# Kernel tuning notes

Hardware: AMD Instinct MI355X
Metric: run time of the kernel (lower is better)

The kernel has to match this reference:

```python
import jax, jax.numpy as jnp
import numpy as np

N, D, U = 8192, 512, 256

def setup_inputs() -> dict:
    key = jax.random.key(0)
    ks = jax.random.split(key, 5)
    s = 0.02
    return {
        "x": jax.random.normal(ks[0], (N, D), dtype=jnp.float32),
        "W_q": jax.random.normal(ks[1], (D, U), dtype=jnp.float32) * s,
        "W_k": jax.random.normal(ks[2], (D, U), dtype=jnp.float32) * s,
        "W_v": jax.random.normal(ks[3], (D, U), dtype=jnp.float32) * s,
        "W_o": jax.random.normal(ks[4], (U, D), dtype=jnp.float32) * s,
    }

def reference(x, W_q, W_k, W_v, W_o):
    # x: [N, d]; attention over the sample (batch) dimension
    units = W_q.shape[-1]
    Q = x @ W_q            # [N, U]
    Km = x @ W_k           # [N, U]
    V = x @ W_v            # [N, U]
    scale = 1.0 / jnp.sqrt(jnp.asarray(units, dtype=x.dtype))
    scores = jax.nn.softmax((Q @ Km.T) * scale, axis=-1)  # [N, N]
    return (scores @ V) @ W_o  # [N, d]
```

## Files before the change

kernel.cpp:

```cpp
#include <hip/hip_runtime.h>
#include <stdint.h>


#define N_ 8192
#define D_ 512
#define U_ 256

typedef __attribute__((ext_vector_type(8))) short short8;
typedef __attribute__((ext_vector_type(4))) float f32x4;
typedef __attribute__((ext_vector_type(16))) float f32x16;
typedef __attribute__((ext_vector_type(4))) unsigned int u32x4;
typedef __attribute__((ext_vector_type(2))) unsigned int u32x2;
typedef __attribute__((ext_vector_type(2))) unsigned int uint2v;

#define EXP2F(x) __builtin_amdgcn_exp2f(x)

static __device__ __forceinline__ unsigned short f2bf(float f) {
    union { float f; unsigned int u; } c; c.f = f;
    unsigned int u = c.u;
    u += 0x7FFFu + ((u >> 16) & 1u);
    return (unsigned short)(u >> 16);
}
static __device__ __forceinline__ float bf2f(unsigned int h) {
    union { unsigned int u; float f; } c; c.u = h << 16;
    return c.f;
}
static __device__ __forceinline__ unsigned int cvtpk(float lo, float hi) {
    unsigned int d;
    asm("v_cvt_pk_bf16_f32 %0, %1, %2" : "=v"(d) : "v"(lo), "v"(hi));
    return d;
}

__global__ void k_convert(const float* __restrict__ x, const float* __restrict__ Wq,
                          const float* __restrict__ Wk, const float* __restrict__ Wv,
                          const float* __restrict__ Wo,
                          unsigned short* __restrict__ Wt, unsigned short* __restrict__ Wot,
                          unsigned short* __restrict__ xb) {
    const int b = blockIdx.x, t = threadIdx.x;
    if (b < 2048) {
        int i = (b * 256 + t) * 8;
        f32x4 a = *(const f32x4*)(x + i);
        f32x4 c = *(const f32x4*)(x + i + 4);
        u32x4 o;
        o[0] = cvtpk(a[0], a[1]); o[1] = cvtpk(a[2], a[3]);
        o[2] = cvtpk(c[0], c[1]); o[3] = cvtpk(c[2], c[3]);
        *(u32x4*)(xb + i) = o;
    } else {
        int idx = (b - 2048) * 256 + t;
        if (idx < 768 * 512) {
            int j = idx >> 9, d = idx & 511;
            int which = j >> 8, u = j & 255;
            const float* W = (which == 0) ? Wq : ((which == 1) ? Wk : Wv);
            float v = W[d * 256 + u];
            if (which == 0) v *= 0.0625f * 1.4426950408889634f;
            Wt[idx] = f2bf(v);
        } else {
            int i2 = idx - 768 * 512;
            int jj = i2 >> 8, u = i2 & 255;
            Wot[i2] = f2bf(Wo[u * 512 + jj]);
        }
    }
}

__global__ __launch_bounds__(256) void k_qkv(const unsigned short* __restrict__ xb,
        const unsigned short* __restrict__ Wt,
        unsigned short* __restrict__ Q, unsigned short* __restrict__ K,
        unsigned short* __restrict__ Vt) {
    __shared__ __align__(16) char lds[65536];

    const int t = threadIdx.x;
    const int w = t >> 6, l = t & 63;
    const int lg = l >> 4, ln = l & 15;
    const int bm = blockIdx.x * 128;
    const int j0 = blockIdx.y * 128;

    const int r8 = t >> 3, c8 = t & 7;
    const char* gA = (const char*)xb + (size_t)bm * 1024;
    const char* gB = (const char*)Wt + (size_t)j0 * 1024;

    auto stage = [&](int ks, int b) {
        const char* ga = gA + ks * 128;
        const char* gb = gB + ks * 128;
        char* la = lds + b * 16384;
        char* lb = lds + 32768 + b * 16384;
#pragma unroll
        for (int i = 0; i < 4; ++i) {
            int row = i * 32 + r8;
            int so = row * 1024 + ((c8 ^ (row & 7)) << 4);
            __builtin_amdgcn_global_load_lds(
                (const __attribute__((address_space(1))) void*)(ga + so),
                (__attribute__((address_space(3))) void*)(la + (i * 256 + t) * 16), 16, 0, 0);
            __builtin_amdgcn_global_load_lds(
                (const __attribute__((address_space(1))) void*)(gb + so),
                (__attribute__((address_space(3))) void*)(lb + (i * 256 + t) * 16), 16, 0, 0);
        }
    };

    f32x4 acc[2][8] = {};
    stage(0, 0);
    for (int ks = 0; ks < 8; ++ks) {
        const int buf = ks & 1;
        __syncthreads();
        if (ks + 1 < 8) stage(ks + 1, buf ^ 1);
        const char* la = lds + buf * 16384;
        const char* lb = lds + 32768 + buf * 16384;
#pragma unroll
        for (int kc = 0; kc < 2; ++kc) {
            short8 af0, af1;
            {
                int ar0 = w * 32 + ln;
                int ar1 = w * 32 + 16 + ln;
                af0 = *(const short8*)(la + ar0 * 128 + (((kc * 4 + lg) ^ (ar0 & 7)) << 4));
                af1 = *(const short8*)(la + ar1 * 128 + (((kc * 4 + lg) ^ (ar1 & 7)) << 4));
            }
#pragma unroll
            for (int jt = 0; jt < 8; ++jt) {
                int br = jt * 16 + ln;
                short8 bf = *(const short8*)(lb + br * 128 + (((kc * 4 + lg) ^ (br & 7)) << 4));
                acc[0][jt] = __builtin_amdgcn_mfma_f32_16x16x32_bf16(af0, bf, acc[0][jt], 0, 0, 0);
                acc[1][jt] = __builtin_amdgcn_mfma_f32_16x16x32_bf16(af1, bf, acc[1][jt], 0, 0, 0);
            }
        }
    }

    if (j0 < 512) {
        unsigned short* dst = (j0 < 256) ? Q : K;
        int jb = (j0 < 256) ? j0 : (j0 - 256);
#pragma unroll
        for (int rt = 0; rt < 2; ++rt)
#pragma unroll
            for (int jt = 0; jt < 8; ++jt)
#pragma unroll
                for (int i = 0; i < 4; ++i)
                    dst[(size_t)(bm + w * 32 + rt * 16 + lg * 4 + i) * U_ + jb + jt * 16 + ln]
                        = f2bf(acc[rt][jt][i]);
    } else {
        __syncthreads();
        short* ldsT = (short*)lds;
#pragma unroll
        for (int rt = 0; rt < 2; ++rt)
#pragma unroll
            for (int jt = 0; jt < 8; ++jt)
#pragma unroll
                for (int i = 0; i < 4; ++i)
                    ldsT[(jt * 16 + ln) * 136 + (w * 32 + rt * 16 + lg * 4 + i)]
                        = (short)f2bf(acc[rt][jt][i]);
        __syncthreads();
        int u = t >> 1, half = t & 1;
        int vrow = (j0 - 512) + u;
#pragma unroll
        for (int s = 0; s < 8; ++s) {
            short8 v = *(const short8*)(&ldsT[u * 136 + half * 64 + s * 8]);
            *(short8*)(Vt + (size_t)vrow * N_ + bm + half * 64 + s * 8) = v;
        }
    }
}

__global__ __launch_bounds__(256, 2) void k_attn(const unsigned short* __restrict__ Qm,
        const unsigned short* __restrict__ Km, const unsigned short* __restrict__ Vt,
        unsigned short* __restrict__ Opart, float* __restrict__ ml) {
    __shared__ __align__(16) char ldsK[2][16384];
    __shared__ __align__(16) char ldsV[2][16384];
    __shared__ float ldsA[4][32];

    const int tid = threadIdx.x;
    const int w = tid >> 6, l = tid & 63;
    const int j31 = l & 31, hi = l >> 5;
    const int sp = blockIdx.x & 7;
    const int bx = blockIdx.x >> 3;
    const int q0w = bx * 128 + w * 32;
    const int jbase = sp * 1024;

    short8 qf[16];
#pragma unroll
    for (int ks = 0; ks < 16; ++ks)
        qf[ks] = *(const short8*)(Qm + (size_t)(q0w + j31) * U_ + ks * 16 + hi * 8);

    f32x16 acc[8] = {};
    float mrun = -3.0e38f, lsum = 0.f;

    const int kbase = j31 * 512 + ((hi ^ (j31 & 1)) << 4);
    const int kxor = (j31 >> 1) & 7;
    const int sK = tid & 31, rK = tid >> 5;

    const int cV = tid & 3, uV = tid >> 2;
    const int swV = (cV ^ ((uV >> 2) & 3)) << 4;
    const int vsw = (j31 >> 2) & 3;
    const int vb0 = j31 * 64 + (((0 + hi) ^ vsw) << 4);
    const int vb1 = j31 * 64 + (((2 + hi) ^ vsw) << 4);

    {
        const char* gV = (const char*)Vt + (size_t)jbase * 2;
        u32x4 rv0 = *(const u32x4*)(gV + (size_t)(uV +   0) * 16384 + cV * 16);
        u32x4 rv1 = *(const u32x4*)(gV + (size_t)(uV +  64) * 16384 + cV * 16);
        u32x4 rv2 = *(const u32x4*)(gV + (size_t)(uV + 128) * 16384 + cV * 16);
        u32x4 rv3 = *(const u32x4*)(gV + (size_t)(uV + 192) * 16384 + cV * 16);
        const char* gK = (const char*)Km + (size_t)jbase * 512;
#pragma unroll
        for (int r = 0; r < 4; ++r) {
            int row = r * 8 + rK;
            const char* src = gK + row * 512 + ((sK ^ (row & 15)) << 4);
            char* dst = &ldsK[0][(row * 32 + sK) * 16];
            __builtin_amdgcn_global_load_lds((const __attribute__((address_space(1))) void*)src,
                                             (__attribute__((address_space(3))) void*)dst, 16, 0, 0);
        }
        char* lv = &ldsV[0][0];
        *(u32x4*)(lv + (uV +   0) * 64 + swV) = rv0;
        *(u32x4*)(lv + (uV +  64) * 64 + swV) = rv1;
        *(u32x4*)(lv + (uV + 128) * 64 + swV) = rv2;
        *(u32x4*)(lv + (uV + 192) * 64 + swV) = rv3;
    }

    for (int it = 0; it < 32; ++it) {
        const int buf = it & 1, nb = buf ^ 1;
        __syncthreads();

        u32x4 rv0, rv1, rv2, rv3;
        const bool more = (it + 1 < 32);
        if (more) {
            const int j1 = jbase + (it + 1) * 32;
            const char* gV = (const char*)Vt + (size_t)j1 * 2;
            rv0 = *(const u32x4*)(gV + (size_t)(uV +   0) * 16384 + cV * 16);
            rv1 = *(const u32x4*)(gV + (size_t)(uV +  64) * 16384 + cV * 16);
            rv2 = *(const u32x4*)(gV + (size_t)(uV + 128) * 16384 + cV * 16);
            rv3 = *(const u32x4*)(gV + (size_t)(uV + 192) * 16384 + cV * 16);
            const char* gK = (const char*)Km + (size_t)j1 * 512;
#pragma unroll
            for (int r = 0; r < 4; ++r) {
                int row = r * 8 + rK;
                const char* src = gK + row * 512 + ((sK ^ (row & 15)) << 4);
                char* dst = &ldsK[nb][(row * 32 + sK) * 16];
                __builtin_amdgcn_global_load_lds((const __attribute__((address_space(1))) void*)src,
                                                 (__attribute__((address_space(3))) void*)dst, 16, 0, 0);
            }
        }

        f32x16 sc = {};
        const char* kb = ldsK[buf] + kbase;
        __builtin_amdgcn_s_setprio(1);
#pragma unroll
        for (int ks = 0; ks < 16; ++ks) {
            short8 kf = *(const short8*)(kb + ((ks ^ kxor) << 5));
            sc = __builtin_amdgcn_mfma_f32_32x32x16_bf16(kf, qf[ks], sc, 0, 0, 0);
        }
        __builtin_amdgcn_s_setprio(0);

        float t0 = fmaxf(fmaxf(fmaxf(sc[0], sc[1]), fmaxf(sc[2], sc[3])),
                         fmaxf(fmaxf(sc[4], sc[5]), fmaxf(sc[6], sc[7])));
        float t1 = fmaxf(fmaxf(fmaxf(sc[8], sc[9]), fmaxf(sc[10], sc[11])),
                         fmaxf(fmaxf(sc[12], sc[13]), fmaxf(sc[14], sc[15])));
        float tmax = fmaxf(t0, t1);
        tmax = fmaxf(tmax, __shfl_xor(tmax, 32, 64));
        int need = (tmax > mrun + 2.0f);
        if (__any(need)) {
            float mnew = fmaxf(mrun, tmax);
            float al = EXP2F(mrun - mnew);
            mrun = mnew;
            lsum *= al;
            if (l < 32) ldsA[w][l] = al;
            asm volatile("s_waitcnt lgkmcnt(0)" ::: "memory");
            __builtin_amdgcn_sched_barrier(0);
#pragma unroll
            for (int t4 = 0; t4 < 4; ++t4) {
                f32x4 av = *(const f32x4*)&ldsA[w][t4 * 8 + hi * 4];
#pragma unroll
                for (int ut = 0; ut < 8; ++ut) {
                    acc[ut][4 * t4 + 0] *= av[0];
                    acc[ut][4 * t4 + 1] *= av[1];
                    acc[ut][4 * t4 + 2] *= av[2];
                    acc[ut][4 * t4 + 3] *= av[3];
                }
            }
        }
#pragma unroll
        for (int r = 0; r < 16; ++r) sc[r] = EXP2F(sc[r] - mrun);
        lsum += ((sc[0] + sc[1]) + (sc[2] + sc[3])) + ((sc[4] + sc[5]) + (sc[6] + sc[7]))
              + ((sc[8] + sc[9]) + (sc[10] + sc[11])) + ((sc[12] + sc[13]) + (sc[14] + sc[15]));

        unsigned int pk0 = cvtpk(sc[0], sc[1]),  pk1 = cvtpk(sc[2], sc[3]);
        unsigned int pk2 = cvtpk(sc[4], sc[5]),  pk3 = cvtpk(sc[6], sc[7]);
        unsigned int pk4 = cvtpk(sc[8], sc[9]),  pk5 = cvtpk(sc[10], sc[11]);
        unsigned int pk6 = cvtpk(sc[12], sc[13]), pk7 = cvtpk(sc[14], sc[15]);
        uint2v r02 = __builtin_amdgcn_permlane32_swap(pk0, pk2, false, false);
        uint2v r13 = __builtin_amdgcn_permlane32_swap(pk1, pk3, false, false);
        uint2v r46 = __builtin_amdgcn_permlane32_swap(pk4, pk6, false, false);
        uint2v r57 = __builtin_amdgcn_permlane32_swap(pk5, pk7, false, false);
        union { u32x4 u; short8 s; } fa0, fa1;
        fa0.u[0] = r02[0]; fa0.u[1] = r13[0]; fa0.u[2] = r02[1]; fa0.u[3] = r13[1];
        fa1.u[0] = r46[0]; fa1.u[1] = r57[0]; fa1.u[2] = r46[1]; fa1.u[3] = r57[1];

        if (more) {
            char* lv = &ldsV[nb][0];
            *(u32x4*)(lv + (uV +   0) * 64 + swV) = rv0;
            *(u32x4*)(lv + (uV +  64) * 64 + swV) = rv1;
            *(u32x4*)(lv + (uV + 128) * 64 + swV) = rv2;
            *(u32x4*)(lv + (uV + 192) * 64 + swV) = rv3;
        }

        const char* vb = ldsV[buf];
        __builtin_amdgcn_s_setprio(1);
#pragma unroll
        for (int ut = 0; ut < 8; ++ut) {
            short8 b0 = *(const short8*)(vb + ut * 2048 + vb0);
            short8 b1 = *(const short8*)(vb + ut * 2048 + vb1);
            acc[ut] = __builtin_amdgcn_mfma_f32_32x32x16_bf16(fa0.s, b0, acc[ut], 0, 0, 0);
            acc[ut] = __builtin_amdgcn_mfma_f32_32x32x16_bf16(fa1.s, b1, acc[ut], 0, 0, 0);
        }
        __builtin_amdgcn_s_setprio(0);
    }

    float ltot = lsum + __shfl_xor(lsum, 32, 64);
    if (l < 32) {
        int row = q0w + l;
        ml[(size_t)sp * 2 * N_ + row]      = mrun;
        ml[(size_t)sp * 2 * N_ + N_ + row] = ltot;
    }
    unsigned int* Op32 = (unsigned int*)(Opart + (size_t)sp * N_ * U_);
    const int unit = bx * 4 + w;
#pragma unroll
    for (int ut = 0; ut < 8; ++ut) {
        unsigned int o[8];
#pragma unroll
        for (int t = 0; t < 8; ++t) o[t] = cvtpk(acc[ut][2 * t], acc[ut][2 * t + 1]);
        unsigned int* dst = Op32 + (size_t)(unit * 4096 + ut * 512 + l * 8);
        *(u32x4*)(dst)     = *(u32x4*)&o[0];
        *(u32x4*)(dst + 4) = *(u32x4*)&o[4];
    }
}

__global__ __launch_bounds__(256) void k_cout(const unsigned short* __restrict__ Opart,
        const float* __restrict__ ml, const unsigned short* __restrict__ Wot,
        float* __restrict__ out) {
    __shared__ float tile[32][260];
    __shared__ float Arow[8][32];
    __shared__ float Linv[32];
    __shared__ unsigned short t16[32][264];
    const int t = threadIdx.x, unit = blockIdx.x;
    const int q0 = unit * 32;

    if (t < 32) {
        float m = -3.0e38f;
#pragma unroll
        for (int sp = 0; sp < 8; ++sp) m = fmaxf(m, ml[(size_t)sp * 2 * N_ + q0 + t]);
        float L = 0.f;
#pragma unroll
        for (int sp = 0; sp < 8; ++sp) {
            float a = EXP2F(ml[(size_t)sp * 2 * N_ + q0 + t] - m);
            Arow[sp][t] = a;
            L += ml[(size_t)sp * 2 * N_ + N_ + q0 + t] * a;
        }
        Linv[t] = 1.0f / L;
    }
    __syncthreads();

    {
        const int qb = 8 * (t & 3) + 4 * (t >> 7);
        const int lane = t >> 2;
        float a0[8], a1[8], a2[8], a3[8];
#pragma unroll
        for (int it = 0; it < 8; ++it) { a0[it] = 0.f; a1[it] = 0.f; a2[it] = 0.f; a3[it] = 0.f; }
        const unsigned int* Ob = (const unsigned int*)Opart;
#pragma unroll
        for (int sp = 0; sp < 8; ++sp) {
            const unsigned int* base = Ob + (size_t)sp * (N_ * U_ / 2) + unit * 4096;
            float w0 = Arow[sp][qb], w1 = Arow[sp][qb + 1], w2 = Arow[sp][qb + 2], w3 = Arow[sp][qb + 3];
#pragma unroll
            for (int it = 0; it < 8; ++it) {
                u32x2 pk = *(const u32x2*)(base + it * 512 + t * 2);
                a0[it] += bf2f(pk[0] & 0xffffu) * w0;
                a1[it] += bf2f(pk[0] >> 16) * w1;
                a2[it] += bf2f(pk[1] & 0xffffu) * w2;
                a3[it] += bf2f(pk[1] >> 16) * w3;
            }
        }
#pragma unroll
        for (int it = 0; it < 8; ++it) {
            int u = it * 32 + (lane & 31);
            tile[qb + 0][u] = a0[it];
            tile[qb + 1][u] = a1[it];
            tile[qb + 2][u] = a2[it];
            tile[qb + 3][u] = a3[it];
        }
    }
    __syncthreads();

    {
        const int row = t >> 3, c0 = (t & 7) * 32;
        float li = Linv[row];
#pragma unroll
        for (int k = 0; k < 32; ++k)
            t16[row][c0 + k] = f2bf(tile[row][c0 + k] * li);
    }
    __syncthreads();

    const int w = t >> 6, l = t & 63;
    const int lg = l >> 4, ln = l & 15;
    const int rt = w & 1;
    const int jh = (w >> 1) * 256;
    f32x4 acc[16] = {};
#pragma unroll
    for (int kc = 0; kc < 8; ++kc) {
        short8 afr = *(const short8*)(&t16[rt * 16 + ln][kc * 32 + 8 * lg]);
#pragma unroll
        for (int jt = 0; jt < 16; ++jt) {
            short8 bfr = *(const short8*)(Wot + (size_t)(jh + 16 * jt + ln) * U_ + kc * 32 + 8 * lg);
            acc[jt] = __builtin_amdgcn_mfma_f32_16x16x32_bf16(afr, bfr, acc[jt], 0, 0, 0);
        }
    }
#pragma unroll
    for (int jt = 0; jt < 16; ++jt)
#pragma unroll
        for (int i = 0; i < 4; ++i)
            out[(size_t)(q0 + rt * 16 + lg * 4 + i) * D_ + jh + 16 * jt + ln] = acc[jt][i];
}

extern "C" void kernel_launch(void* const* d_in, const int* in_sizes, int n_in,
                              void* d_out, int out_size, void* d_ws, size_t ws_size,
                              hipStream_t stream) {
    const float* x  = (const float*)d_in[0];
    const float* Wq = (const float*)d_in[1];
    const float* Wk = (const float*)d_in[2];
    const float* Wv = (const float*)d_in[3];
    const float* Wo = (const float*)d_in[4];
    float* out = (float*)d_out;

    char* ws = (char*)d_ws;
    unsigned short* Wt    = (unsigned short*)(ws);
    unsigned short* Wot   = (unsigned short*)(ws + 786432);
    unsigned short* xb    = (unsigned short*)(ws + 1048576);
    unsigned short* Q     = (unsigned short*)(ws + 9437184);
    unsigned short* K     = (unsigned short*)(ws + 13631488);
    unsigned short* Vt    = (unsigned short*)(ws + 17825792);
    unsigned short* Opart = (unsigned short*)(ws + 26214400);
    float*          mlp   = (float*)(ws + 59768832);
    (void)in_sizes; (void)n_in; (void)out_size; (void)ws_size;

    k_convert<<<4096, 256, 0, stream>>>(x, Wq, Wk, Wv, Wo, Wt, Wot, xb);
    k_qkv<<<dim3(64, 6), 256, 0, stream>>>(xb, Wt, Q, K, Vt);
    k_attn<<<512, 256, 0, stream>>>(Q, K, Vt, Opart, mlp);
    k_cout<<<256, 256, 0, stream>>>(Opart, mlp, Wot, out);
}
```

Measured before the change: 155.9 us.

## Double k_cout threads, pack V transpose LDS stores, reshape max reduction

The output-projection kernel k_cout now runs 512 threads per block instead of 256. Each thread handles half the partial-combine iterations, half the normalisation columns and half the output column tiles, which is meant to raise parallelism and cut per-thread latency across its 256 blocks. The V-transpose epilogue in k_qkv packs four bf16 values into one 64-bit LDS store instead of four scalar stores. The row-max reduction in k_attn is regrouped into three-input fmax chains, likely so the compiler can emit max3 instructions. These changes cost more register pressure per block and a different LDS access pattern.

```diff
diff --git a/kernel.cpp b/kernel.cpp
--- a/kernel.cpp
+++ b/kernel.cpp
@@ -140,11 +140,12 @@
 #pragma unroll
         for (int rt = 0; rt < 2; ++rt)
 #pragma unroll
-            for (int jt = 0; jt < 8; ++jt)
-#pragma unroll
-                for (int i = 0; i < 4; ++i)
-                    ldsT[(jt * 16 + ln) * 136 + (w * 32 + rt * 16 + lg * 4 + i)]
-                        = (short)f2bf(acc[rt][jt][i]);
+            for (int jt = 0; jt < 8; ++jt) {
+                u32x2 p;
+                p[0] = cvtpk(acc[rt][jt][0], acc[rt][jt][1]);
+                p[1] = cvtpk(acc[rt][jt][2], acc[rt][jt][3]);
+                *(u32x2*)(&ldsT[(jt * 16 + ln) * 136 + (w * 32 + rt * 16 + lg * 4)]) = p;
+            }
         __syncthreads();
         int u = t >> 1, half = t & 1;
         int vrow = (j0 - 512) + u;
@@ -245,11 +246,14 @@
         }
         __builtin_amdgcn_s_setprio(0);
 
-        float t0 = fmaxf(fmaxf(fmaxf(sc[0], sc[1]), fmaxf(sc[2], sc[3])),
-                         fmaxf(fmaxf(sc[4], sc[5]), fmaxf(sc[6], sc[7])));
-        float t1 = fmaxf(fmaxf(fmaxf(sc[8], sc[9]), fmaxf(sc[10], sc[11])),
-                         fmaxf(fmaxf(sc[12], sc[13]), fmaxf(sc[14], sc[15])));
-        float tmax = fmaxf(t0, t1);
+        float a3_ = fmaxf(fmaxf(sc[0], sc[1]), sc[2]);
+        float b3_ = fmaxf(fmaxf(sc[3], sc[4]), sc[5]);
+        float c3_ = fmaxf(fmaxf(sc[6], sc[7]), sc[8]);
+        float d3_ = fmaxf(fmaxf(sc[9], sc[10]), sc[11]);
+        float e3_ = fmaxf(fmaxf(sc[12], sc[13]), sc[14]);
+        float f3_ = fmaxf(fmaxf(a3_, b3_), c3_);
+        float g3_ = fmaxf(fmaxf(d3_, e3_), sc[15]);
+        float tmax = fmaxf(f3_, g3_);
         tmax = fmaxf(tmax, __shfl_xor(tmax, 32, 64));
         int need = (tmax > mrun + 2.0f);
         if (__any(need)) {
@@ -328,7 +332,7 @@
     }
 }
 
-__global__ __launch_bounds__(256) void k_cout(const unsigned short* __restrict__ Opart,
+__global__ __launch_bounds__(512) void k_cout(const unsigned short* __restrict__ Opart,
         const float* __restrict__ ml, const unsigned short* __restrict__ Wot,
         float* __restrict__ out) {
     __shared__ float tile[32][260];
@@ -354,19 +358,21 @@
     __syncthreads();
 
     {
-        const int qb = 8 * (t & 3) + 4 * (t >> 7);
-        const int lane = t >> 2;
-        float a0[8], a1[8], a2[8], a3[8];
-#pragma unroll
-        for (int it = 0; it < 8; ++it) { a0[it] = 0.f; a1[it] = 0.f; a2[it] = 0.f; a3[it] = 0.f; }
+        const int tb = t & 255;
+        const int qb = 8 * (tb & 3) + 4 * (tb >> 7);
+        const int lane = tb >> 2;
+        const int it0 = (t >> 8) * 4;
+        float a0[4], a1[4], a2[4], a3[4];
+#pragma unroll
+        for (int it = 0; it < 4; ++it) { a0[it] = 0.f; a1[it] = 0.f; a2[it] = 0.f; a3[it] = 0.f; }
         const unsigned int* Ob = (const unsigned int*)Opart;
 #pragma unroll
         for (int sp = 0; sp < 8; ++sp) {
             const unsigned int* base = Ob + (size_t)sp * (N_ * U_ / 2) + unit * 4096;
             float w0 = Arow[sp][qb], w1 = Arow[sp][qb + 1], w2 = Arow[sp][qb + 2], w3 = Arow[sp][qb + 3];
 #pragma unroll
-            for (int it = 0; it < 8; ++it) {
-                u32x2 pk = *(const u32x2*)(base + it * 512 + t * 2);
+            for (int it = 0; it < 4; ++it) {
+                u32x2 pk = *(const u32x2*)(base + (it0 + it) * 512 + tb * 2);
                 a0[it] += bf2f(pk[0] & 0xffffu) * w0;
                 a1[it] += bf2f(pk[0] >> 16) * w1;
                 a2[it] += bf2f(pk[1] & 0xffffu) * w2;
@@ -374,8 +380,8 @@
             }
         }
 #pragma unroll
-        for (int it = 0; it < 8; ++it) {
-            int u = it * 32 + (lane & 31);
+        for (int it = 0; it < 4; ++it) {
+            int u = (it0 + it) * 32 + (lane & 31);
             tile[qb + 0][u] = a0[it];
             tile[qb + 1][u] = a1[it];
             tile[qb + 2][u] = a2[it];
@@ -385,10 +391,10 @@
     __syncthreads();
 
     {
-        const int row = t >> 3, c0 = (t & 7) * 32;
+        const int row = t >> 4, c0 = (t & 15) * 16;
         float li = Linv[row];
 #pragma unroll
-        for (int k = 0; k < 32; ++k)
+        for (int k = 0; k < 16; ++k)
             t16[row][c0 + k] = f2bf(tile[row][c0 + k] * li);
     }
     __syncthreads();
@@ -396,19 +402,19 @@
     const int w = t >> 6, l = t & 63;
     const int lg = l >> 4, ln = l & 15;
     const int rt = w & 1;
-    const int jh = (w >> 1) * 256;
-    f32x4 acc[16] = {};
+    const int jh = (w >> 1) * 128;
+    f32x4 acc[8] = {};
 #pragma unroll
     for (int kc = 0; kc < 8; ++kc) {
         short8 afr = *(const short8*)(&t16[rt * 16 + ln][kc * 32 + 8 * lg]);
 #pragma unroll
-        for (int jt = 0; jt < 16; ++jt) {
+        for (int jt = 0; jt < 8; ++jt) {
             short8 bfr = *(const short8*)(Wot + (size_t)(jh + 16 * jt + ln) * U_ + kc * 32 + 8 * lg);
             acc[jt] = __builtin_amdgcn_mfma_f32_16x16x32_bf16(afr, bfr, acc[jt], 0, 0, 0);
         }
     }
 #pragma unroll
-    for (int jt = 0; jt < 16; ++jt)
+    for (int jt = 0; jt < 8; ++jt)
 #pragma unroll
         for (int i = 0; i < 4; ++i)
             out[(size_t)(q0 + rt * 16 + lg * 4 + i) * D_ + jh + 16 * jt + ln] = acc[jt][i];
@@ -438,5 +444,5 @@
     k_convert<<<4096, 256, 0, stream>>>(x, Wq, Wk, Wv, Wo, Wt, Wot, xb);
     k_qkv<<<dim3(64, 6), 256, 0, stream>>>(xb, Wt, Q, K, Vt);
     k_attn<<<512, 256, 0, stream>>>(Q, K, Vt, Opart, mlp);
-    k_cout<<<256, 256, 0, stream>>>(Opart, mlp, Wot, out);
-}
+    k_cout<<<256, 512, 0, stream>>>(Opart, mlp, Wot, out);
+}
```

After: 152.8 us (median of 2 runs). 2.0% less time.
